# Optimization experiments

Measured on AMD Instinct MI355X. Metric: run time of the kernel, lower is better.

Reference implementation:

```python
import jax, jax.numpy as jnp
import numpy as np

B, N_P, N_S = 64, 50, 200
N_NODES = N_P * N_S          # 10000 nodes per graph (jobs x ops)
N_CAND = N_S + 1             # 201 candidates
INPUT_DIM, HIDDEN = 3, 64
NODE_DIM = 2 * HIDDEN        # h_nodes feature dim (=> actor in = 6*HIDDEN)
POOL_DIM = 4 * HIDDEN        # h_pooled dim (mean || max pooling)
H_ACTOR, H_CRITIC = 256, 256


def setup_inputs() -> dict:
    key = jax.random.key(0)
    ks = jax.random.split(key, 16)
    p = lambda k, sh: jax.random.normal(k, sh, jnp.float32) * 0.02
    x = jax.random.normal(ks[0], (B, N_NODES, INPUT_DIM), jnp.float32)
    candidate = jax.random.randint(ks[1], (B, N_CAND), 0, N_NODES)
    mask = jax.random.randint(ks[2], (B, N_CAND), 0, 2) > 0
    mask = mask.at[:, 0].set(True)  # guarantee at least one valid action per row
    return {
        "x": x, "candidate": candidate, "mask": mask,
        "fe_w1": p(ks[3], (INPUT_DIM, HIDDEN)), "fe_b1": jnp.zeros((HIDDEN,), jnp.float32),
        "fe_w2": p(ks[4], (HIDDEN, NODE_DIM)), "fe_b2": jnp.zeros((NODE_DIM,), jnp.float32),
        "a_w1": p(ks[5], (NODE_DIM + POOL_DIM, H_ACTOR)), "a_b1": jnp.zeros((H_ACTOR,), jnp.float32),
        "a_w2": p(ks[6], (H_ACTOR, H_ACTOR)), "a_b2": jnp.zeros((H_ACTOR,), jnp.float32),
        "a_w3": p(ks[7], (H_ACTOR, 1)), "a_b3": jnp.zeros((1,), jnp.float32),
        "c_w1": p(ks[8], (POOL_DIM, H_CRITIC)), "c_b1": jnp.zeros((H_CRITIC,), jnp.float32),
        "c_w2": p(ks[9], (H_CRITIC, H_CRITIC)), "c_b2": jnp.zeros((H_CRITIC,), jnp.float32),
        "c_w3": p(ks[10], (H_CRITIC, 1)), "c_b3": jnp.zeros((1,), jnp.float32),
    }


def _actor_critic(x, candidate, mask,
                  fe_w1, fe_b1, fe_w2, fe_b2,
                  a_w1, a_b1, a_w2, a_b2, a_w3, a_b3,
                  c_w1, c_b1, c_w2, c_b2, c_w3, c_b3):
    # --- feature_extract: per-node MLP embedding, graph-level pooling ---
    h = jax.nn.relu(jnp.einsum('bni,ih->bnh', x, fe_w1) + fe_b1)
    h_nodes = jax.nn.relu(jnp.einsum('bnh,hd->bnd', h, fe_w2) + fe_b2)   # [B, N, 2H]
    h_pooled = jnp.concatenate([h_nodes.mean(axis=1), h_nodes.max(axis=1)], axis=-1)  # [B, 4H]

    # --- gather candidate node features (torch.gather over node axis) ---
    cand_feat = jnp.take_along_axis(h_nodes, candidate[:, :, None], axis=1)  # [B, C, 2H]

    # --- concat broadcast pooled feature ---
    pooled_rep = jnp.broadcast_to(h_pooled[:, None, :], (cand_feat.shape[0], cand_feat.shape[1], h_pooled.shape[-1]))
    concat_fea = jnp.concatenate([cand_feat, pooled_rep], axis=-1)  # [B, C, 6H]

    # --- actor MLP (tanh hidden layers, linear out) ---
    a = jnp.tanh(concat_fea @ a_w1 + a_b1)
    a = jnp.tanh(a @ a_w2 + a_b2)
    scores = a @ a_w3 + a_b3                                    # [B, C, 1]

    # --- mask with -inf, softmax over candidate axis ---
    scores = jnp.where(mask[:, :, None], scores, -jnp.inf)
    pi = jax.nn.softmax(scores, axis=1)                          # [B, C, 1]

    # --- critic MLP on pooled feature ---
    c = jnp.tanh(h_pooled @ c_w1 + c_b1)
    c = jnp.tanh(c @ c_w2 + c_b2)
    v = c @ c_w3 + c_b3                                          # [B, 1]
    return pi, v


def reference(x, candidate, mask,
              fe_w1, fe_b1, fe_w2, fe_b2,
              a_w1, a_b1, a_w2, a_b2, a_w3, a_b3,
              c_w1, c_b1, c_w2, c_b2, c_w3, c_b3):
    return _actor_critic(x, candidate, mask,
                         fe_w1, fe_b1, fe_w2, fe_b2,
                         a_w1, a_b1, a_w2, a_b2, a_w3, a_b3,
                         c_w1, c_b1, c_w2, c_b2, c_w3, c_b3)
```

## Files before the change

### kernel.cpp

```cpp
#include <hip/hip_runtime.h>

#define NN 10000
#define NCAND 201
#define NB 64

typedef __attribute__((ext_vector_type(8))) short short8;
typedef __attribute__((ext_vector_type(4))) float f32x4;

__device__ __forceinline__ float bf2f(unsigned short u) {
  return __uint_as_float(((unsigned int)u) << 16);
}
__device__ __forceinline__ unsigned short f2bf(float f) {
  unsigned int u = __float_as_uint(f);
  u += 0x7FFFu + ((u >> 16) & 1u);
  return (unsigned short)(u >> 16);
}
__device__ __forceinline__ float fast_tanh(float x) {
  return 1.0f - 2.0f / (__expf(2.0f * x) + 1.0f);
}
__device__ __forceinline__ float gld(const void* p, long i, int f) {
  return f ? ((const float*)p)[i] : bf2f(((const unsigned short*)p)[i]);
}

__global__ __launch_bounds__(256)
void prep_kernel(const void* x, const void* w1, const void* b1, const void* w2,
                 const void* b2, const void* aw1, const void* ab1, const void* aw2,
                 const void* ab2, const void* aw3, const void* ab3,
                 const void* cw1, const void* cb1, const void* cw2, const void* cb2,
                 const void* cw3, const void* cb3,
                 const unsigned int* mask_w, const unsigned int* cand_w,
                 int* F, float* zero_base,
                 unsigned short* __restrict__ w2t, unsigned short* __restrict__ aw1t,
                 unsigned short* __restrict__ aw2t,
                 unsigned short* __restrict__ cw1t, unsigned short* __restrict__ cw2t) {
  const int t = threadIdx.x;
  const int j = blockIdx.x;

  if (j < 384) {
    __shared__ int cnts[5];
    if (t < 5) cnts[t] = 0;
    __syncthreads();
    const void* aps[5] = {w2, aw1, aw2, cw1, cw2};
#pragma unroll
    for (int a = 0; a < 5; ++a) {
      const unsigned short* p = (const unsigned short*)aps[a];
      if ((p[t] & 0x7F80u) >= 0x4300u) atomicAdd(&cnts[a], 1);
    }
    __syncthreads();
    const int Fw2 = cnts[0] > 32, Faw1 = cnts[1] > 32, Faw2 = cnts[2] > 32;
    const int Fcw1 = cnts[3] > 32, Fcw2 = cnts[4] > 32;
    int i = j * 256 + t;
    if (i < 128 * 64) { int n = i >> 6, k = i & 63; w2t[i] = f2bf(gld(w2, k * 128 + n, Fw2)); }
    if (i < 256 * 384) { int n = i / 384, k = i % 384; aw1t[i] = f2bf(gld(aw1, k * 256 + n, Faw1)); }
    if (i < 256 * 256) {
      int n = i >> 8, k = i & 255;
      aw2t[i] = f2bf(gld(aw2, k * 256 + n, Faw2));
      cw1t[i] = f2bf(gld(cw1, k * 256 + n, Fcw1));
      cw2t[i] = f2bf(gld(cw2, k * 256 + n, Fcw2));
    }
    return;
  }

  __shared__ int sh[3];
  if (t < 3) sh[t] = 0;
  __syncthreads();

  if (j < 401) {
    const void* ptrs[17] = {x, w1, b1, w2, b2, aw1, ab1, aw2, ab2, aw3, ab3,
                            cw1, cb1, cw2, cb2, cw3, cb3};
    const int sizes[17] = {1920000, 192, 64, 8192, 128, 98304, 256, 65536, 256,
                           256, 1, 65536, 256, 65536, 256, 256, 1};
    int a = j - 384;
    const unsigned short* p = (const unsigned short*)ptrs[a];
    int K = min(sizes[a], 2048);
    int c = 0;
    for (int i = t; i < K; i += 256)
      if ((p[i] & 0x7F80u) >= 0x4300u) c++;
    if (c) atomicAdd(&sh[0], c);
    __syncthreads();
    if (t == 0) F[a] = (sh[0] > (K >> 3)) ? 1 : 0;
  } else if (j == 401) {
    int flo = 0, fhi = 0, fgt = 0;
    for (int i = t; i < 3216; i += 256) {
      unsigned int w = mask_w[i];
      if ((w & 0xFFFFu) == 0x3F80u) flo = 1;
      if ((w >> 16) == 0x3F80u) fhi = 1;
      if (w > 1u) fgt = 1;
    }
    if (flo) sh[0] = 1;
    if (fhi) sh[1] = 1;
    if (fgt) sh[2] = 1;
    __syncthreads();
    if (t == 0) F[17] = sh[0] ? 2 : (sh[1] ? 3 : (sh[2] ? 1 : 0));
  } else if (j == 402) {
    int co = 0;
    for (int i = t; i < 1024; i += 256)
      if ((i & 1) && cand_w[i] != 0u) co = 1;
    if (co) sh[0] = 1;
    __syncthreads();
    if (t == 0) F[18] = sh[0] ? 0 : 1;
  } else {
    zero_base[(j - 403) * 256 + t] = 0.f;
  }
}

__global__ __launch_bounds__(256, 4)
void feat_pool_kernel(const void* __restrict__ x,
                      const void* __restrict__ w1, const void* __restrict__ b1,
                      const unsigned short* __restrict__ w2t,
                      const void* __restrict__ b2,
                      const int* __restrict__ F,
                      float* __restrict__ psum, float* __restrict__ pmax) {
  __shared__ __align__(16) unsigned short h1s[128 * 72];
  __shared__ float w1f[3 * 64];
  __shared__ float b1f[64];
  __shared__ float b2f[128];

  const int t = threadIdx.x;
  const int b = blockIdx.x >> 4;
  const int s = blockIdx.x & 15;
  const int lane = t & 63;
  const int wv = t >> 6;
  const int F0 = F[0], F1 = F[1], F2 = F[2], F4 = F[4];

  if (t < 192) w1f[t] = gld(w1, t, F1);
  if (t < 64) b1f[t] = gld(b1, t, F2);
  if (t < 128) b2f[t] = gld(b2, t, F4);

  short8 bfr[2][2];
#pragma unroll
  for (int nl = 0; nl < 2; ++nl)
#pragma unroll
    for (int ks = 0; ks < 2; ++ks) {
      int col = wv * 32 + nl * 16 + (lane & 15);
      bfr[nl][ks] = *(const short8*)(w2t + col * 64 + ((lane >> 4) * 8) + ks * 32);
    }
  __syncthreads();

  float csum[2] = {0.f, 0.f};
  float cmax[2] = {0.f, 0.f};

  const int m = t & 127;
  const int kg = t >> 7;

  float x0 = 0.f, x1 = 0.f, x2 = 0.f;
  {
    int c0 = s;
    if (c0 < 79) {
      int nb = c0 * 128;
      if (m < min(128, NN - nb)) {
        long xo = ((long)b * NN + nb + m) * 3;
        x0 = gld(x, xo, F0); x1 = gld(x, xo + 1, F0); x2 = gld(x, xo + 2, F0);
      }
    }
  }

  for (int c = s; c < 79; c += 16) {
    int nb = c * 128;
    int cnt = (nb + 128 <= NN) ? 128 : (NN - nb);
    if (m < cnt) {
#pragma unroll
      for (int blk = 0; blk < 4; ++blk) {
        short8 v;
#pragma unroll
        for (int i = 0; i < 8; ++i) {
          int k = kg * 32 + blk * 8 + i;
          float vv = x0 * w1f[k] + x1 * w1f[64 + k] + x2 * w1f[128 + k] + b1f[k];
          v[i] = (short)f2bf(fmaxf(vv, 0.f));
        }
        *(short8*)(h1s + m * 72 + kg * 32 + blk * 8) = v;
      }
    }
    {
      int cn = c + 16;
      float nx0 = 0.f, nx1 = 0.f, nx2 = 0.f;
      if (cn < 79) {
        int nbn = cn * 128;
        if (m < min(128, NN - nbn)) {
          long xo = ((long)b * NN + nbn + m) * 3;
          nx0 = gld(x, xo, F0); nx1 = gld(x, xo + 1, F0); nx2 = gld(x, xo + 2, F0);
        }
      }
      __syncthreads();
      x0 = nx0; x1 = nx1; x2 = nx2;
    }
#pragma unroll
    for (int mt = 0; mt < 8; ++mt) {
      const unsigned short* ap = h1s + (mt * 16 + (lane & 15)) * 72 + ((lane >> 4) * 8);
      short8 af0 = *(const short8*)(ap);
      short8 af1 = *(const short8*)(ap + 32);
#pragma unroll
      for (int nl = 0; nl < 2; ++nl) {
        f32x4 acc = {0.f, 0.f, 0.f, 0.f};
        acc = __builtin_amdgcn_mfma_f32_16x16x32_bf16(af0, bfr[nl][0], acc, 0, 0, 0);
        acc = __builtin_amdgcn_mfma_f32_16x16x32_bf16(af1, bfr[nl][1], acc, 0, 0, 0);
        int col = wv * 32 + nl * 16 + (lane & 15);
        float bb = b2f[col];
#pragma unroll
        for (int r = 0; r < 4; ++r) {
          int row = mt * 16 + ((lane >> 4) * 4) + r;
          if (row < cnt) {
            float v = fmaxf(acc[r] + bb, 0.f);
            csum[nl] += v;
            cmax[nl] = fmaxf(cmax[nl], v);
          }
        }
      }
    }
    __syncthreads();
  }
#pragma unroll
  for (int nl = 0; nl < 2; ++nl) {
    csum[nl] += __shfl_xor(csum[nl], 16);
    csum[nl] += __shfl_xor(csum[nl], 32);
    cmax[nl] = fmaxf(cmax[nl], __shfl_xor(cmax[nl], 16));
    cmax[nl] = fmaxf(cmax[nl], __shfl_xor(cmax[nl], 32));
  }
  if (lane < 16) {
#pragma unroll
    for (int nl = 0; nl < 2; ++nl) {
      int col = wv * 32 + nl * 16 + lane;
      atomicAdd(&psum[b * 128 + col], csum[nl]);
      atomicMax((int*)&pmax[b * 128 + col], __float_as_int(cmax[nl]));
    }
  }
}

__global__ __launch_bounds__(256)
void pooled_proj_kernel(const float* __restrict__ psum, const float* __restrict__ pmax,
                        const unsigned short* __restrict__ aw1t,
                        const void* __restrict__ ab1, const int* __restrict__ F,
                        float* __restrict__ pact) {
  __shared__ float plf[256];
  const int t = threadIdx.x, b = blockIdx.x;
  const int F6 = F[6];
  if (t < 128) {
    plf[t] = bf2f(f2bf(psum[b * 128 + t] * (1.0f / 10000.0f)));
    plf[128 + t] = bf2f(f2bf(pmax[b * 128 + t]));
  }
  __syncthreads();
  float a = gld(ab1, t, F6);
  const unsigned short* row = aw1t + t * 384 + 128;
#pragma unroll
  for (int k8 = 0; k8 < 32; ++k8) {
    short8 w = *(const short8*)(row + k8 * 8);
#pragma unroll
    for (int j = 0; j < 8; ++j)
      a += plf[k8 * 8 + j] * bf2f((unsigned short)w[j]);
  }
  pact[b * 256 + t] = a;
}

__global__ __launch_bounds__(256)
void actor_kernel(const void* __restrict__ x, const int* __restrict__ cand,
                  const void* __restrict__ w1, const void* __restrict__ b1,
                  const void* __restrict__ b2bf,
                  const void* __restrict__ ab2,
                  const void* __restrict__ aw3, const void* __restrict__ ab3,
                  const int* __restrict__ F,
                  const float* __restrict__ pact,
                  const unsigned short* __restrict__ w2t,
                  const unsigned short* __restrict__ aw1t,
                  const unsigned short* __restrict__ aw2t,
                  float* __restrict__ scores) {
  __shared__ __align__(16) unsigned short h1c[32 * 72];
  __shared__ __align__(16) unsigned short cf[32 * 136];
  __shared__ __align__(16) unsigned short a1s[32 * 264];
  __shared__ __align__(16) unsigned short a2s[32 * 264];
  __shared__ float pactS[256], ab2f[256], b2f[128];

  const int t = threadIdx.x;
  const int b = blockIdx.x / 7;
  const int cb = blockIdx.x % 7;
  const int cbase = cb * 29;
  const int cntc = min(29, NCAND - cbase);
  const int lane = t & 63;
  const int wv = t >> 6;
  const int F0 = F[0], F1 = F[1], F2 = F[2], F4 = F[4], F8 = F[8];
  const int F9 = F[9], F10 = F[10], C64 = F[18];

  pactS[t] = pact[b * 256 + t];
  ab2f[t] = gld(ab2, t, F8);
  if (t < 128) b2f[t] = gld(b2bf, t, F4);

  {
    int r = t & 31;
    int ci = cbase + r;
    if (ci > NCAND - 1) ci = NCAND - 1;
    long cidx = (long)b * NCAND + ci;
    int nd = C64 ? cand[2 * cidx] : cand[cidx];
    long xo = ((long)b * NN + nd) * 3;
    float x0 = gld(x, xo, F0), x1 = gld(x, xo + 1, F0), x2 = gld(x, xo + 2, F0);
    int kg = t >> 5;
#pragma unroll
    for (int i = 0; i < 8; ++i) {
      int k = kg * 8 + i;
      float v = x0 * gld(w1, k, F1) + x1 * gld(w1, 64 + k, F1) +
                x2 * gld(w1, 128 + k, F1) + gld(b1, k, F2);
      h1c[r * 72 + k] = f2bf(fmaxf(v, 0.f));
    }
  }
  __syncthreads();

  {
    short8 af[2][2];
#pragma unroll
    for (int mt = 0; mt < 2; ++mt)
#pragma unroll
      for (int ks = 0; ks < 2; ++ks)
        af[mt][ks] = *(const short8*)(h1c + (mt * 16 + (lane & 15)) * 72 + ((lane >> 4) * 8) + ks * 32);
#pragma unroll
    for (int nl = 0; nl < 2; ++nl) {
      int col = wv * 32 + nl * 16 + (lane & 15);
      short8 bf0 = *(const short8*)(w2t + col * 64 + ((lane >> 4) * 8));
      short8 bf1 = *(const short8*)(w2t + col * 64 + ((lane >> 4) * 8) + 32);
      float bb = b2f[col];
#pragma unroll
      for (int mt = 0; mt < 2; ++mt) {
        f32x4 acc = {0.f, 0.f, 0.f, 0.f};
        acc = __builtin_amdgcn_mfma_f32_16x16x32_bf16(af[mt][0], bf0, acc, 0, 0, 0);
        acc = __builtin_amdgcn_mfma_f32_16x16x32_bf16(af[mt][1], bf1, acc, 0, 0, 0);
#pragma unroll
        for (int r = 0; r < 4; ++r) {
          int row = mt * 16 + ((lane >> 4) * 4) + r;
          cf[row * 136 + col] = f2bf(fmaxf(acc[r] + bb, 0.f));
        }
      }
    }
  }
  __syncthreads();

  {
    f32x4 acc[2][4];
#pragma unroll
    for (int mt = 0; mt < 2; ++mt)
#pragma unroll
      for (int nt = 0; nt < 4; ++nt) acc[mt][nt] = (f32x4){0.f, 0.f, 0.f, 0.f};
#pragma unroll
    for (int ks = 0; ks < 4; ++ks) {
      short8 af0 = *(const short8*)(cf + (lane & 15) * 136 + ks * 32 + ((lane >> 4) * 8));
      short8 af1 = *(const short8*)(cf + (16 + (lane & 15)) * 136 + ks * 32 + ((lane >> 4) * 8));
#pragma unroll
      for (int nt = 0; nt < 4; ++nt) {
        int col = wv * 64 + nt * 16 + (lane & 15);
        short8 bfr = *(const short8*)(aw1t + col * 384 + ks * 32 + ((lane >> 4) * 8));
        acc[0][nt] = __builtin_amdgcn_mfma_f32_16x16x32_bf16(af0, bfr, acc[0][nt], 0, 0, 0);
        acc[1][nt] = __builtin_amdgcn_mfma_f32_16x16x32_bf16(af1, bfr, acc[1][nt], 0, 0, 0);
      }
    }
#pragma unroll
    for (int mt = 0; mt < 2; ++mt)
#pragma unroll
      for (int nt = 0; nt < 4; ++nt) {
        int col = wv * 64 + nt * 16 + (lane & 15);
        float bb = pactS[col];
#pragma unroll
        for (int r = 0; r < 4; ++r) {
          int row = mt * 16 + ((lane >> 4) * 4) + r;
          a1s[row * 264 + col] = f2bf(fast_tanh(acc[mt][nt][r] + bb));
        }
      }
  }
  __syncthreads();

  {
    f32x4 acc[2][4];
#pragma unroll
    for (int mt = 0; mt < 2; ++mt)
#pragma unroll
      for (int nt = 0; nt < 4; ++nt) acc[mt][nt] = (f32x4){0.f, 0.f, 0.f, 0.f};
    for (int ks = 0; ks < 8; ++ks) {
      short8 af0 = *(const short8*)(a1s + (lane & 15) * 264 + ks * 32 + ((lane >> 4) * 8));
      short8 af1 = *(const short8*)(a1s + (16 + (lane & 15)) * 264 + ks * 32 + ((lane >> 4) * 8));
#pragma unroll
      for (int nt = 0; nt < 4; ++nt) {
        int col = wv * 64 + nt * 16 + (lane & 15);
        short8 bfr = *(const short8*)(aw2t + col * 256 + ks * 32 + ((lane >> 4) * 8));
        acc[0][nt] = __builtin_amdgcn_mfma_f32_16x16x32_bf16(af0, bfr, acc[0][nt], 0, 0, 0);
        acc[1][nt] = __builtin_amdgcn_mfma_f32_16x16x32_bf16(af1, bfr, acc[1][nt], 0, 0, 0);
      }
    }
#pragma unroll
    for (int mt = 0; mt < 2; ++mt)
#pragma unroll
      for (int nt = 0; nt < 4; ++nt) {
        int col = wv * 64 + nt * 16 + (lane & 15);
        float bb = ab2f[col];
#pragma unroll
        for (int r = 0; r < 4; ++r) {
          int row = mt * 16 + ((lane >> 4) * 4) + r;
          a2s[row * 264 + col] = f2bf(fast_tanh(acc[mt][nt][r] + bb));
        }
      }
  }
  __syncthreads();

  {
    int row = t >> 3, seg = t & 7;
    float p = 0.f;
#pragma unroll 8
    for (int i = 0; i < 32; ++i) {
      int k = seg * 32 + i;
      p += bf2f(a2s[row * 264 + k]) * gld(aw3, k, F9);
    }
    p += __shfl_xor(p, 1);
    p += __shfl_xor(p, 2);
    p += __shfl_xor(p, 4);
    if (seg == 0 && row < cntc)
      scores[b * 256 + cbase + row] = p + gld(ab3, 0, F10);
  }
}

__global__ __launch_bounds__(256)
void softmax_critic_kernel(const float* __restrict__ scores,
                           const void* __restrict__ mask,
                           const int* __restrict__ F,
                           const float* __restrict__ psum,
                           const float* __restrict__ pmax,
                           const unsigned short* __restrict__ cw1t,
                           const unsigned short* __restrict__ cw2t,
                           const void* __restrict__ cb1, const void* __restrict__ cb2,
                           const void* __restrict__ cw3, const void* __restrict__ cb3,
                           void* __restrict__ out) {
  __shared__ float plf[256];
  __shared__ float c1f[256];
  __shared__ float red[4];
  const int t = threadIdx.x;
  const int b = blockIdx.x & 63;
  const int lane = t & 63, wv = t >> 6;
  const int OF = (F[0] + F[1] + F[3] + F[5] + F[7] + F[9] + F[11] + F[13] + F[15]) >= 5;

  if (blockIdx.x < 64) {
    const int MM = F[17];
    float sraw = 0.f, sv = -1e30f;
    bool valid = false;
    if (t < NCAND) {
      sraw = scores[b * 256 + t];
      long idx = (long)b * NCAND + t;
      if (MM == 0)      valid = ((const int*)mask)[idx] != 0;
      else if (MM == 1) valid = ((const unsigned char*)mask)[idx] != 0;
      else if (MM == 2) valid = ((const unsigned short*)mask)[idx] != 0;
      else              valid = ((const unsigned int*)mask)[idx] != 0;
      if (valid) sv = sraw;
    }
    float m = sv;
    for (int o = 32; o; o >>= 1) m = fmaxf(m, __shfl_xor(m, o));
    if (lane == 0) red[wv] = m;
    __syncthreads();
    m = fmaxf(fmaxf(red[0], red[1]), fmaxf(red[2], red[3]));
    __syncthreads();
    float e = valid ? __expf(sraw - m) : 0.f;
    if (!(e == e)) e = 0.f;
    float ss = e;
    for (int o = 32; o; o >>= 1) ss += __shfl_xor(ss, o);
    if (lane == 0) red[wv] = ss;
    __syncthreads();
    float tot = red[0] + red[1] + red[2] + red[3];
    tot = fmaxf(tot, 1e-30f);
    if (t < NCAND) {
      float pv = e / tot;
      if (!(pv == pv)) pv = 0.f;
      if (OF) ((float*)out)[b * NCAND + t] = pv;
      else ((unsigned short*)out)[b * NCAND + t] = f2bf(pv);
    }
  } else {
    const int F12 = F[12], F14 = F[14], F15 = F[15], F16 = F[16];
    if (t < 128) {
      plf[t] = psum[b * 128 + t] * (1.0f / 10000.0f);
      plf[128 + t] = pmax[b * 128 + t];
    }
    __syncthreads();
    {
      float a = gld(cb1, t, F12);
      const unsigned short* row = cw1t + t * 256;
#pragma unroll
      for (int k8 = 0; k8 < 32; ++k8) {
        short8 w = *(const short8*)(row + k8 * 8);
#pragma unroll
        for (int j = 0; j < 8; ++j)
          a += plf[k8 * 8 + j] * bf2f((unsigned short)w[j]);
      }
      c1f[t] = fast_tanh(a);
    }
    __syncthreads();
    {
      float a2 = gld(cb2, t, F14);
      const unsigned short* row = cw2t + t * 256;
#pragma unroll
      for (int k8 = 0; k8 < 32; ++k8) {
        short8 w = *(const short8*)(row + k8 * 8);
#pragma unroll
        for (int j = 0; j < 8; ++j)
          a2 += c1f[k8 * 8 + j] * bf2f((unsigned short)w[j]);
      }
      a2 = fast_tanh(a2);
      float p = a2 * gld(cw3, t, F15);
      for (int o = 32; o; o >>= 1) p += __shfl_xor(p, o);
      __syncthreads();
      if (lane == 0) red[wv] = p;
      __syncthreads();
      if (t == 0) {
        float v = red[0] + red[1] + red[2] + red[3] + gld(cb3, 0, F16);
        if (!(v == v)) v = 0.f;
        if (OF) ((float*)out)[NB * NCAND + b] = v;
        else ((unsigned short*)out)[NB * NCAND + b] = f2bf(v);
      }
    }
  }
}

extern "C" void kernel_launch(void* const* d_in, const int* in_sizes, int n_in,
                              void* d_out, int out_size, void* d_ws, size_t ws_size,
                              hipStream_t stream) {
  const void* x = d_in[0];
  const int* cand = (const int*)d_in[1];
  const void* mask = d_in[2];
  const void* fe_w1 = d_in[3];
  const void* fe_b1 = d_in[4];
  const void* fe_w2 = d_in[5];
  const void* fe_b2 = d_in[6];
  const void* a_w1 = d_in[7];
  const void* a_b1 = d_in[8];
  const void* a_w2 = d_in[9];
  const void* a_b2 = d_in[10];
  const void* a_w3 = d_in[11];
  const void* a_b3 = d_in[12];
  const void* c_w1 = d_in[13];
  const void* c_b1 = d_in[14];
  const void* c_w2 = d_in[15];
  const void* c_b2 = d_in[16];
  const void* c_w3 = d_in[17];
  const void* c_b3 = d_in[18];

  char* ws = (char*)d_ws;
  float* psum = (float*)(ws + 0);
  float* pmax = (float*)(ws + 32768);
  float* scores = (float*)(ws + 65536);
  unsigned short* w2t = (unsigned short*)(ws + 131072);
  unsigned short* aw1t = (unsigned short*)(ws + 147456);
  unsigned short* aw2t = (unsigned short*)(ws + 344064);
  int* F = (int*)(ws + 475136);
  unsigned short* cw1t = (unsigned short*)(ws + 475264);
  unsigned short* cw2t = (unsigned short*)(ws + 606336);
  float* pact = (float*)(ws + 737408);

  prep_kernel<<<467, 256, 0, stream>>>(x, fe_w1, fe_b1, fe_w2, fe_b2,
                                       a_w1, a_b1, a_w2, a_b2, a_w3, a_b3,
                                       c_w1, c_b1, c_w2, c_b2, c_w3, c_b3,
                                       (const unsigned int*)mask,
                                       (const unsigned int*)cand, F, psum,
                                       w2t, aw1t, aw2t, cw1t, cw2t);
  feat_pool_kernel<<<1024, 256, 0, stream>>>(x, fe_w1, fe_b1, w2t, fe_b2, F, psum, pmax);
  pooled_proj_kernel<<<64, 256, 0, stream>>>(psum, pmax, aw1t, a_b1, F, pact);
  actor_kernel<<<448, 256, 0, stream>>>(x, cand, fe_w1, fe_b1, fe_b2,
                                        a_b2, a_w3, a_b3, F, pact,
                                        w2t, aw1t, aw2t, scores);
  softmax_critic_kernel<<<128, 256, 0, stream>>>(scores, mask, F, psum, pmax,
                                                 cw1t, cw2t, c_b1, c_b2, c_w3, c_b3,
                                                 (void*)d_out);
}
```

Baseline: 167.2 us.

## Merge feature pooling with candidate embedding and fuse softmax into actor tail

Candidate node embedding (second feature-extract layer) now runs as extra blocks inside the pooling kernel and writes its bf16 features to workspace. The pooled projection and critic share one kernel. The actor MLP kernel finishes with a last-block-per-batch softmax driven by an atomic counter. This cuts five launches to four and lets the candidate gather overlap with pooling, at the cost of a global round trip for candidate features, atomics, and a serialized softmax tail.

```diff
diff --git a/kernel.cpp b/kernel.cpp
--- a/kernel.cpp
+++ b/kernel.cpp
@@ -29,7 +29,7 @@
                  const void* cw1, const void* cb1, const void* cw2, const void* cb2,
                  const void* cw3, const void* cb3,
                  const unsigned int* mask_w, const unsigned int* cand_w,
-                 int* F, float* zero_base,
+                 int* F, float* zero_base, int* scnt,
                  unsigned short* __restrict__ w2t, unsigned short* __restrict__ aw1t,
                  unsigned short* __restrict__ aw2t,
                  unsigned short* __restrict__ cw1t, unsigned short* __restrict__ cw2t) {
@@ -97,6 +97,7 @@
     for (int i = t; i < 1024; i += 256)
       if ((i & 1) && cand_w[i] != 0u) co = 1;
     if (co) sh[0] = 1;
+    if (t < 64) scnt[t] = 0;
     __syncthreads();
     if (t == 0) F[18] = sh[0] ? 0 : 1;
   } else {
@@ -105,365 +106,220 @@
 }
 
 __global__ __launch_bounds__(256, 4)
-void feat_pool_kernel(const void* __restrict__ x,
+void fp_actorA_kernel(const void* __restrict__ x, const int* __restrict__ cand,
                       const void* __restrict__ w1, const void* __restrict__ b1,
                       const unsigned short* __restrict__ w2t,
                       const void* __restrict__ b2,
                       const int* __restrict__ F,
-                      float* __restrict__ psum, float* __restrict__ pmax) {
-  __shared__ __align__(16) unsigned short h1s[128 * 72];
+                      float* __restrict__ psum, float* __restrict__ pmax,
+                      unsigned short* __restrict__ cfw) {
+  __shared__ __align__(16) unsigned short pool[128 * 72];
   __shared__ float w1f[3 * 64];
   __shared__ float b1f[64];
   __shared__ float b2f[128];
 
   const int t = threadIdx.x;
-  const int b = blockIdx.x >> 4;
-  const int s = blockIdx.x & 15;
   const int lane = t & 63;
   const int wv = t >> 6;
   const int F0 = F[0], F1 = F[1], F2 = F[2], F4 = F[4];
 
-  if (t < 192) w1f[t] = gld(w1, t, F1);
-  if (t < 64) b1f[t] = gld(b1, t, F2);
-  if (t < 128) b2f[t] = gld(b2, t, F4);
-
-  short8 bfr[2][2];
-#pragma unroll
-  for (int nl = 0; nl < 2; ++nl)
-#pragma unroll
-    for (int ks = 0; ks < 2; ++ks) {
-      int col = wv * 32 + nl * 16 + (lane & 15);
-      bfr[nl][ks] = *(const short8*)(w2t + col * 64 + ((lane >> 4) * 8) + ks * 32);
-    }
-  __syncthreads();
-
-  float csum[2] = {0.f, 0.f};
-  float cmax[2] = {0.f, 0.f};
-
-  const int m = t & 127;
-  const int kg = t >> 7;
-
-  float x0 = 0.f, x1 = 0.f, x2 = 0.f;
-  {
-    int c0 = s;
-    if (c0 < 79) {
-      int nb = c0 * 128;
+  if (blockIdx.x < 1024) {
+    unsigned short* h1s = pool;
+    const int b = blockIdx.x >> 4;
+    const int s = blockIdx.x & 15;
+
+    if (t < 192) w1f[t] = gld(w1, t, F1);
+    if (t < 64) b1f[t] = gld(b1, t, F2);
+    if (t < 128) b2f[t] = gld(b2, t, F4);
+
+    short8 bfr[2][2];
+#pragma unroll
+    for (int nl = 0; nl < 2; ++nl)
+#pragma unroll
+      for (int ks = 0; ks < 2; ++ks) {
+        int col = wv * 32 + nl * 16 + (lane & 15);
+        bfr[nl][ks] = *(const short8*)(w2t + col * 64 + ((lane >> 4) * 8) + ks * 32);
+      }
+    __syncthreads();
+
+    float csum[2] = {0.f, 0.f};
+    float cmax[2] = {0.f, 0.f};
+    const int m = t & 127;
+    const int kg = t >> 7;
+
+    float x0 = 0.f, x1 = 0.f, x2 = 0.f;
+    if (s < 79) {
+      int nb = s * 128;
       if (m < min(128, NN - nb)) {
         long xo = ((long)b * NN + nb + m) * 3;
         x0 = gld(x, xo, F0); x1 = gld(x, xo + 1, F0); x2 = gld(x, xo + 2, F0);
       }
     }
-  }
-
-  for (int c = s; c < 79; c += 16) {
-    int nb = c * 128;
-    int cnt = (nb + 128 <= NN) ? 128 : (NN - nb);
-    if (m < cnt) {
-#pragma unroll
-      for (int blk = 0; blk < 4; ++blk) {
-        short8 v;
-#pragma unroll
-        for (int i = 0; i < 8; ++i) {
-          int k = kg * 32 + blk * 8 + i;
-          float vv = x0 * w1f[k] + x1 * w1f[64 + k] + x2 * w1f[128 + k] + b1f[k];
-          v[i] = (short)f2bf(fmaxf(vv, 0.f));
+
+    for (int c = s; c < 79; c += 16) {
+      int nb = c * 128;
+      int cnt = (nb + 128 <= NN) ? 128 : (NN - nb);
+      if (m < cnt) {
+#pragma unroll
+        for (int blk = 0; blk < 4; ++blk) {
+          short8 v;
+#pragma unroll
+          for (int i = 0; i < 8; ++i) {
+            int k = kg * 32 + blk * 8 + i;
+            float vv = x0 * w1f[k] + x1 * w1f[64 + k] + x2 * w1f[128 + k] + b1f[k];
+            v[i] = (short)f2bf(fmaxf(vv, 0.f));
+          }
+          *(short8*)(h1s + m * 72 + kg * 32 + blk * 8) = v;
         }
-        *(short8*)(h1s + m * 72 + kg * 32 + blk * 8) = v;
-      }
-    }
-    {
-      int cn = c + 16;
-      float nx0 = 0.f, nx1 = 0.f, nx2 = 0.f;
-      if (cn < 79) {
-        int nbn = cn * 128;
-        if (m < min(128, NN - nbn)) {
-          long xo = ((long)b * NN + nbn + m) * 3;
-          nx0 = gld(x, xo, F0); nx1 = gld(x, xo + 1, F0); nx2 = gld(x, xo + 2, F0);
-        }
-      }
-      __syncthreads();
-      x0 = nx0; x1 = nx1; x2 = nx2;
-    }
-#pragma unroll
-    for (int mt = 0; mt < 8; ++mt) {
-      const unsigned short* ap = h1s + (mt * 16 + (lane & 15)) * 72 + ((lane >> 4) * 8);
-      short8 af0 = *(const short8*)(ap);
-      short8 af1 = *(const short8*)(ap + 32);
-#pragma unroll
-      for (int nl = 0; nl < 2; ++nl) {
-        f32x4 acc = {0.f, 0.f, 0.f, 0.f};
-        acc = __builtin_amdgcn_mfma_f32_16x16x32_bf16(af0, bfr[nl][0], acc, 0, 0, 0);
-        acc = __builtin_amdgcn_mfma_f32_16x16x32_bf16(af1, bfr[nl][1], acc, 0, 0, 0);
-        int col = wv * 32 + nl * 16 + (lane & 15);
-        float bb = b2f[col];
-#pragma unroll
-        for (int r = 0; r < 4; ++r) {
-          int row = mt * 16 + ((lane >> 4) * 4) + r;
-          if (row < cnt) {
-            float v = fmaxf(acc[r] + bb, 0.f);
-            csum[nl] += v;
-            cmax[nl] = fmaxf(cmax[nl], v);
+      }
+      {
+        int cn = c + 16;
+        float nx0 = 0.f, nx1 = 0.f, nx2 = 0.f;
+        if (cn < 79) {
+          int nbn = cn * 128;
+          if (m < min(128, NN - nbn)) {
+            long xo = ((long)b * NN + nbn + m) * 3;
+            nx0 = gld(x, xo, F0); nx1 = gld(x, xo + 1, F0); nx2 = gld(x, xo + 2, F0);
           }
         }
-      }
-    }
-    __syncthreads();
-  }
-#pragma unroll
-  for (int nl = 0; nl < 2; ++nl) {
-    csum[nl] += __shfl_xor(csum[nl], 16);
-    csum[nl] += __shfl_xor(csum[nl], 32);
-    cmax[nl] = fmaxf(cmax[nl], __shfl_xor(cmax[nl], 16));
-    cmax[nl] = fmaxf(cmax[nl], __shfl_xor(cmax[nl], 32));
-  }
-  if (lane < 16) {
+        __syncthreads();
+        x0 = nx0; x1 = nx1; x2 = nx2;
+      }
+#pragma unroll
+      for (int mt = 0; mt < 8; ++mt) {
+        const unsigned short* ap = h1s + (mt * 16 + (lane & 15)) * 72 + ((lane >> 4) * 8);
+        short8 af0 = *(const short8*)(ap);
+        short8 af1 = *(const short8*)(ap + 32);
+#pragma unroll
+        for (int nl = 0; nl < 2; ++nl) {
+          f32x4 acc = {0.f, 0.f, 0.f, 0.f};
+          acc = __builtin_amdgcn_mfma_f32_16x16x32_bf16(af0, bfr[nl][0], acc, 0, 0, 0);
+          acc = __builtin_amdgcn_mfma_f32_16x16x32_bf16(af1, bfr[nl][1], acc, 0, 0, 0);
+          int col = wv * 32 + nl * 16 + (lane & 15);
+          float bb = b2f[col];
+#pragma unroll
+          for (int r = 0; r < 4; ++r) {
+            int row = mt * 16 + ((lane >> 4) * 4) + r;
+            if (row < cnt) {
+              float v = fmaxf(acc[r] + bb, 0.f);
+              csum[nl] += v;
+              cmax[nl] = fmaxf(cmax[nl], v);
+            }
+          }
+        }
+      }
+      __syncthreads();
+    }
 #pragma unroll
     for (int nl = 0; nl < 2; ++nl) {
-      int col = wv * 32 + nl * 16 + lane;
-      atomicAdd(&psum[b * 128 + col], csum[nl]);
-      atomicMax((int*)&pmax[b * 128 + col], __float_as_int(cmax[nl]));
+      csum[nl] += __shfl_xor(csum[nl], 16);
+      csum[nl] += __shfl_xor(csum[nl], 32);
+      cmax[nl] = fmaxf(cmax[nl], __shfl_xor(cmax[nl], 16));
+      cmax[nl] = fmaxf(cmax[nl], __shfl_xor(cmax[nl], 32));
+    }
+    if (lane < 16) {
+#pragma unroll
+      for (int nl = 0; nl < 2; ++nl) {
+        int col = wv * 32 + nl * 16 + lane;
+        atomicAdd(&psum[b * 128 + col], csum[nl]);
+        atomicMax((int*)&pmax[b * 128 + col], __float_as_int(cmax[nl]));
+      }
+    }
+  } else {
+    unsigned short* h1c = pool;
+    unsigned short* cf = pool + 2560;
+    const int idx = blockIdx.x - 1024;
+    const int b = idx / 7;
+    const int cb = idx % 7;
+    const int cbase = cb * 29;
+    const int C64 = F[18];
+
+    if (t < 128) b2f[t] = gld(b2, t, F4);
+
+    {
+      int r = t & 31;
+      int ci = cbase + r;
+      if (ci > NCAND - 1) ci = NCAND - 1;
+      long cidx = (long)b * NCAND + ci;
+      int nd = C64 ? cand[2 * cidx] : cand[cidx];
+      long xo = ((long)b * NN + nd) * 3;
+      float x0 = gld(x, xo, F0), x1 = gld(x, xo + 1, F0), x2 = gld(x, xo + 2, F0);
+      int kg = t >> 5;
+#pragma unroll
+      for (int i = 0; i < 8; ++i) {
+        int k = kg * 8 + i;
+        float v = x0 * gld(w1, k, F1) + x1 * gld(w1, 64 + k, F1) +
+                  x2 * gld(w1, 128 + k, F1) + gld(b1, k, F2);
+        h1c[r * 72 + k] = f2bf(fmaxf(v, 0.f));
+      }
+    }
+    __syncthreads();
+
+    {
+      short8 af[2][2];
+#pragma unroll
+      for (int mt = 0; mt < 2; ++mt)
+#pragma unroll
+        for (int ks = 0; ks < 2; ++ks)
+          af[mt][ks] = *(const short8*)(h1c + (mt * 16 + (lane & 15)) * 72 + ((lane >> 4) * 8) + ks * 32);
+#pragma unroll
+      for (int nl = 0; nl < 2; ++nl) {
+        int col = wv * 32 + nl * 16 + (lane & 15);
+        short8 bf0 = *(const short8*)(w2t + col * 64 + ((lane >> 4) * 8));
+        short8 bf1 = *(const short8*)(w2t + col * 64 + ((lane >> 4) * 8) + 32);
+        float bb = b2f[col];
+#pragma unroll
+        for (int mt = 0; mt < 2; ++mt) {
+          f32x4 acc = {0.f, 0.f, 0.f, 0.f};
+          acc = __builtin_amdgcn_mfma_f32_16x16x32_bf16(af[mt][0], bf0, acc, 0, 0, 0);
+          acc = __builtin_amdgcn_mfma_f32_16x16x32_bf16(af[mt][1], bf1, acc, 0, 0, 0);
+#pragma unroll
+          for (int r = 0; r < 4; ++r) {
+            int row = mt * 16 + ((lane >> 4) * 4) + r;
+            cfw[(long)idx * 4096 + row * 128 + col] = f2bf(fmaxf(acc[r] + bb, 0.f));
+          }
+        }
+      }
     }
   }
 }
 
 __global__ __launch_bounds__(256)
-void pooled_proj_kernel(const float* __restrict__ psum, const float* __restrict__ pmax,
-                        const unsigned short* __restrict__ aw1t,
-                        const void* __restrict__ ab1, const int* __restrict__ F,
-                        float* __restrict__ pact) {
-  __shared__ float plf[256];
-  const int t = threadIdx.x, b = blockIdx.x;
-  const int F6 = F[6];
-  if (t < 128) {
-    plf[t] = bf2f(f2bf(psum[b * 128 + t] * (1.0f / 10000.0f)));
-    plf[128 + t] = bf2f(f2bf(pmax[b * 128 + t]));
-  }
-  __syncthreads();
-  float a = gld(ab1, t, F6);
-  const unsigned short* row = aw1t + t * 384 + 128;
-#pragma unroll
-  for (int k8 = 0; k8 < 32; ++k8) {
-    short8 w = *(const short8*)(row + k8 * 8);
-#pragma unroll
-    for (int j = 0; j < 8; ++j)
-      a += plf[k8 * 8 + j] * bf2f((unsigned short)w[j]);
-  }
-  pact[b * 256 + t] = a;
-}
-
-__global__ __launch_bounds__(256)
-void actor_kernel(const void* __restrict__ x, const int* __restrict__ cand,
-                  const void* __restrict__ w1, const void* __restrict__ b1,
-                  const void* __restrict__ b2bf,
-                  const void* __restrict__ ab2,
-                  const void* __restrict__ aw3, const void* __restrict__ ab3,
-                  const int* __restrict__ F,
-                  const float* __restrict__ pact,
-                  const unsigned short* __restrict__ w2t,
-                  const unsigned short* __restrict__ aw1t,
-                  const unsigned short* __restrict__ aw2t,
-                  float* __restrict__ scores) {
-  __shared__ __align__(16) unsigned short h1c[32 * 72];
-  __shared__ __align__(16) unsigned short cf[32 * 136];
-  __shared__ __align__(16) unsigned short a1s[32 * 264];
-  __shared__ __align__(16) unsigned short a2s[32 * 264];
-  __shared__ float pactS[256], ab2f[256], b2f[128];
-
-  const int t = threadIdx.x;
-  const int b = blockIdx.x / 7;
-  const int cb = blockIdx.x % 7;
-  const int cbase = cb * 29;
-  const int cntc = min(29, NCAND - cbase);
-  const int lane = t & 63;
-  const int wv = t >> 6;
-  const int F0 = F[0], F1 = F[1], F2 = F[2], F4 = F[4], F8 = F[8];
-  const int F9 = F[9], F10 = F[10], C64 = F[18];
-
-  pactS[t] = pact[b * 256 + t];
-  ab2f[t] = gld(ab2, t, F8);
-  if (t < 128) b2f[t] = gld(b2bf, t, F4);
-
-  {
-    int r = t & 31;
-    int ci = cbase + r;
-    if (ci > NCAND - 1) ci = NCAND - 1;
-    long cidx = (long)b * NCAND + ci;
-    int nd = C64 ? cand[2 * cidx] : cand[cidx];
-    long xo = ((long)b * NN + nd) * 3;
-    float x0 = gld(x, xo, F0), x1 = gld(x, xo + 1, F0), x2 = gld(x, xo + 2, F0);
-    int kg = t >> 5;
-#pragma unroll
-    for (int i = 0; i < 8; ++i) {
-      int k = kg * 8 + i;
-      float v = x0 * gld(w1, k, F1) + x1 * gld(w1, 64 + k, F1) +
-                x2 * gld(w1, 128 + k, F1) + gld(b1, k, F2);
-      h1c[r * 72 + k] = f2bf(fmaxf(v, 0.f));
-    }
-  }
-  __syncthreads();
-
-  {
-    short8 af[2][2];
-#pragma unroll
-    for (int mt = 0; mt < 2; ++mt)
-#pragma unroll
-      for (int ks = 0; ks < 2; ++ks)
-        af[mt][ks] = *(const short8*)(h1c + (mt * 16 + (lane & 15)) * 72 + ((lane >> 4) * 8) + ks * 32);
-#pragma unroll
-    for (int nl = 0; nl < 2; ++nl) {
-      int col = wv * 32 + nl * 16 + (lane & 15);
-      short8 bf0 = *(const short8*)(w2t + col * 64 + ((lane >> 4) * 8));
-      short8 bf1 = *(const short8*)(w2t + col * 64 + ((lane >> 4) * 8) + 32);
-      float bb = b2f[col];
-#pragma unroll
-      for (int mt = 0; mt < 2; ++mt) {
-        f32x4 acc = {0.f, 0.f, 0.f, 0.f};
-        acc = __builtin_amdgcn_mfma_f32_16x16x32_bf16(af[mt][0], bf0, acc, 0, 0, 0);
-        acc = __builtin_amdgcn_mfma_f32_16x16x32_bf16(af[mt][1], bf1, acc, 0, 0, 0);
-#pragma unroll
-        for (int r = 0; r < 4; ++r) {
-          int row = mt * 16 + ((lane >> 4) * 4) + r;
-          cf[row * 136 + col] = f2bf(fmaxf(acc[r] + bb, 0.f));
-        }
-      }
-    }
-  }
-  __syncthreads();
-
-  {
-    f32x4 acc[2][4];
-#pragma unroll
-    for (int mt = 0; mt < 2; ++mt)
-#pragma unroll
-      for (int nt = 0; nt < 4; ++nt) acc[mt][nt] = (f32x4){0.f, 0.f, 0.f, 0.f};
-#pragma unroll
-    for (int ks = 0; ks < 4; ++ks) {
-      short8 af0 = *(const short8*)(cf + (lane & 15) * 136 + ks * 32 + ((lane >> 4) * 8));
-      short8 af1 = *(const short8*)(cf + (16 + (lane & 15)) * 136 + ks * 32 + ((lane >> 4) * 8));
-#pragma unroll
-      for (int nt = 0; nt < 4; ++nt) {
-        int col = wv * 64 + nt * 16 + (lane & 15);
-        short8 bfr = *(const short8*)(aw1t + col * 384 + ks * 32 + ((lane >> 4) * 8));
-        acc[0][nt] = __builtin_amdgcn_mfma_f32_16x16x32_bf16(af0, bfr, acc[0][nt], 0, 0, 0);
-        acc[1][nt] = __builtin_amdgcn_mfma_f32_16x16x32_bf16(af1, bfr, acc[1][nt], 0, 0, 0);
-      }
-    }
-#pragma unroll
-    for (int mt = 0; mt < 2; ++mt)
-#pragma unroll
-      for (int nt = 0; nt < 4; ++nt) {
-        int col = wv * 64 + nt * 16 + (lane & 15);
-        float bb = pactS[col];
-#pragma unroll
-        for (int r = 0; r < 4; ++r) {
-          int row = mt * 16 + ((lane >> 4) * 4) + r;
-          a1s[row * 264 + col] = f2bf(fast_tanh(acc[mt][nt][r] + bb));
-        }
-      }
-  }
-  __syncthreads();
-
-  {
-    f32x4 acc[2][4];
-#pragma unroll
-    for (int mt = 0; mt < 2; ++mt)
-#pragma unroll
-      for (int nt = 0; nt < 4; ++nt) acc[mt][nt] = (f32x4){0.f, 0.f, 0.f, 0.f};
-    for (int ks = 0; ks < 8; ++ks) {
-      short8 af0 = *(const short8*)(a1s + (lane & 15) * 264 + ks * 32 + ((lane >> 4) * 8));
-      short8 af1 = *(const short8*)(a1s + (16 + (lane & 15)) * 264 + ks * 32 + ((lane >> 4) * 8));
-#pragma unroll
-      for (int nt = 0; nt < 4; ++nt) {
-        int col = wv * 64 + nt * 16 + (lane & 15);
-        short8 bfr = *(const short8*)(aw2t + col * 256 + ks * 32 + ((lane >> 4) * 8));
-        acc[0][nt] = __builtin_amdgcn_mfma_f32_16x16x32_bf16(af0, bfr, acc[0][nt], 0, 0, 0);
-        acc[1][nt] = __builtin_amdgcn_mfma_f32_16x16x32_bf16(af1, bfr, acc[1][nt], 0, 0, 0);
-      }
-    }
-#pragma unroll
-    for (int mt = 0; mt < 2; ++mt)
-#pragma unroll
-      for (int nt = 0; nt < 4; ++nt) {
-        int col = wv * 64 + nt * 16 + (lane & 15);
-        float bb = ab2f[col];
-#pragma unroll
-        for (int r = 0; r < 4; ++r) {
-          int row = mt * 16 + ((lane >> 4) * 4) + r;
-          a2s[row * 264 + col] = f2bf(fast_tanh(acc[mt][nt][r] + bb));
-        }
-      }
-  }
-  __syncthreads();
-
-  {
-    int row = t >> 3, seg = t & 7;
-    float p = 0.f;
-#pragma unroll 8
-    for (int i = 0; i < 32; ++i) {
-      int k = seg * 32 + i;
-      p += bf2f(a2s[row * 264 + k]) * gld(aw3, k, F9);
-    }
-    p += __shfl_xor(p, 1);
-    p += __shfl_xor(p, 2);
-    p += __shfl_xor(p, 4);
-    if (seg == 0 && row < cntc)
-      scores[b * 256 + cbase + row] = p + gld(ab3, 0, F10);
-  }
-}
-
-__global__ __launch_bounds__(256)
-void softmax_critic_kernel(const float* __restrict__ scores,
-                           const void* __restrict__ mask,
-                           const int* __restrict__ F,
-                           const float* __restrict__ psum,
-                           const float* __restrict__ pmax,
-                           const unsigned short* __restrict__ cw1t,
-                           const unsigned short* __restrict__ cw2t,
-                           const void* __restrict__ cb1, const void* __restrict__ cb2,
-                           const void* __restrict__ cw3, const void* __restrict__ cb3,
-                           void* __restrict__ out) {
+void pp_critic_kernel(const float* __restrict__ psum, const float* __restrict__ pmax,
+                      const unsigned short* __restrict__ aw1t,
+                      const void* __restrict__ ab1,
+                      const unsigned short* __restrict__ cw1t,
+                      const unsigned short* __restrict__ cw2t,
+                      const void* __restrict__ cb1, const void* __restrict__ cb2,
+                      const void* __restrict__ cw3, const void* __restrict__ cb3,
+                      const int* __restrict__ F,
+                      float* __restrict__ pact, void* __restrict__ out) {
   __shared__ float plf[256];
   __shared__ float c1f[256];
   __shared__ float red[4];
   const int t = threadIdx.x;
   const int b = blockIdx.x & 63;
   const int lane = t & 63, wv = t >> 6;
-  const int OF = (F[0] + F[1] + F[3] + F[5] + F[7] + F[9] + F[11] + F[13] + F[15]) >= 5;
 
   if (blockIdx.x < 64) {
-    const int MM = F[17];
-    float sraw = 0.f, sv = -1e30f;
-    bool valid = false;
-    if (t < NCAND) {
-      sraw = scores[b * 256 + t];
-      long idx = (long)b * NCAND + t;
-      if (MM == 0)      valid = ((const int*)mask)[idx] != 0;
-      else if (MM == 1) valid = ((const unsigned char*)mask)[idx] != 0;
-      else if (MM == 2) valid = ((const unsigned short*)mask)[idx] != 0;
-      else              valid = ((const unsigned int*)mask)[idx] != 0;
-      if (valid) sv = sraw;
-    }
-    float m = sv;
-    for (int o = 32; o; o >>= 1) m = fmaxf(m, __shfl_xor(m, o));
-    if (lane == 0) red[wv] = m;
-    __syncthreads();
-    m = fmaxf(fmaxf(red[0], red[1]), fmaxf(red[2], red[3]));
-    __syncthreads();
-    float e = valid ? __expf(sraw - m) : 0.f;
-    if (!(e == e)) e = 0.f;
-    float ss = e;
-    for (int o = 32; o; o >>= 1) ss += __shfl_xor(ss, o);
-    if (lane == 0) red[wv] = ss;
-    __syncthreads();
-    float tot = red[0] + red[1] + red[2] + red[3];
-    tot = fmaxf(tot, 1e-30f);
-    if (t < NCAND) {
-      float pv = e / tot;
-      if (!(pv == pv)) pv = 0.f;
-      if (OF) ((float*)out)[b * NCAND + t] = pv;
-      else ((unsigned short*)out)[b * NCAND + t] = f2bf(pv);
-    }
+    const int F6 = F[6];
+    if (t < 128) {
+      plf[t] = bf2f(f2bf(psum[b * 128 + t] * (1.0f / 10000.0f)));
+      plf[128 + t] = bf2f(f2bf(pmax[b * 128 + t]));
+    }
+    __syncthreads();
+    float a = gld(ab1, t, F6);
+    const unsigned short* row = aw1t + t * 384 + 128;
+#pragma unroll
+    for (int k8 = 0; k8 < 32; ++k8) {
+      short8 w = *(const short8*)(row + k8 * 8);
+#pragma unroll
+      for (int j = 0; j < 8; ++j)
+        a += plf[k8 * 8 + j] * bf2f((unsigned short)w[j]);
+    }
+    pact[b * 256 + t] = a;
   } else {
+    const int OF = (F[0] + F[1] + F[3] + F[5] + F[7] + F[9] + F[11] + F[13] + F[15]) >= 5;
     const int F12 = F[12], F14 = F[14], F15 = F[15], F16 = F[16];
     if (t < 128) {
       plf[t] = psum[b * 128 + t] * (1.0f / 10000.0f);
@@ -506,6 +362,160 @@
         else ((unsigned short*)out)[NB * NCAND + b] = f2bf(v);
       }
     }
+  }
+}
+
+__global__ __launch_bounds__(256)
+void actorB_kernel(const unsigned short* __restrict__ cfw,
+                   const void* __restrict__ ab2,
+                   const void* __restrict__ aw3, const void* __restrict__ ab3,
+                   const void* __restrict__ mask,
+                   const int* __restrict__ F,
+                   const float* __restrict__ pact,
+                   const unsigned short* __restrict__ aw1t,
+                   const unsigned short* __restrict__ aw2t,
+                   float* __restrict__ scores, int* __restrict__ scnt,
+                   void* __restrict__ out) {
+  __shared__ __align__(16) unsigned short a1s[32 * 264];
+  __shared__ __align__(16) unsigned short a2s[32 * 264];
+  __shared__ float pactS[256], ab2f[256];
+  __shared__ float red[4];
+  __shared__ int amLast;
+
+  const int t = threadIdx.x;
+  const int b = blockIdx.x / 7;
+  const int cb = blockIdx.x % 7;
+  const int cbase = cb * 29;
+  const int cntc = min(29, NCAND - cbase);
+  const int lane = t & 63;
+  const int wv = t >> 6;
+  const int F8 = F[8], F9 = F[9], F10 = F[10];
+
+  pactS[t] = pact[b * 256 + t];
+  ab2f[t] = gld(ab2, t, F8);
+
+  {
+    f32x4 acc[2][4];
+#pragma unroll
+    for (int mt = 0; mt < 2; ++mt)
+#pragma unroll
+      for (int nt = 0; nt < 4; ++nt) acc[mt][nt] = (f32x4){0.f, 0.f, 0.f, 0.f};
+    const unsigned short* cfb = cfw + (long)blockIdx.x * 4096;
+#pragma unroll
+    for (int ks = 0; ks < 4; ++ks) {
+      short8 af0 = *(const short8*)(cfb + (lane & 15) * 128 + ks * 32 + ((lane >> 4) * 8));
+      short8 af1 = *(const short8*)(cfb + (16 + (lane & 15)) * 128 + ks * 32 + ((lane >> 4) * 8));
+#pragma unroll
+      for (int nt = 0; nt < 4; ++nt) {
+        int col = wv * 64 + nt * 16 + (lane & 15);
+        short8 bfr = *(const short8*)(aw1t + col * 384 + ks * 32 + ((lane >> 4) * 8));
+        acc[0][nt] = __builtin_amdgcn_mfma_f32_16x16x32_bf16(af0, bfr, acc[0][nt], 0, 0, 0);
+        acc[1][nt] = __builtin_amdgcn_mfma_f32_16x16x32_bf16(af1, bfr, acc[1][nt], 0, 0, 0);
+      }
+    }
+    __syncthreads();
+#pragma unroll
+    for (int mt = 0; mt < 2; ++mt)
+#pragma unroll
+      for (int nt = 0; nt < 4; ++nt) {
+        int col = wv * 64 + nt * 16 + (lane & 15);
+        float bb = pactS[col];
+#pragma unroll
+        for (int r = 0; r < 4; ++r) {
+          int row = mt * 16 + ((lane >> 4) * 4) + r;
+          a1s[row * 264 + col] = f2bf(fast_tanh(acc[mt][nt][r] + bb));
+        }
+      }
+  }
+  __syncthreads();
+
+  {
+    f32x4 acc[2][4];
+#pragma unroll
+    for (int mt = 0; mt < 2; ++mt)
+#pragma unroll
+      for (int nt = 0; nt < 4; ++nt) acc[mt][nt] = (f32x4){0.f, 0.f, 0.f, 0.f};
+    for (int ks = 0; ks < 8; ++ks) {
+      short8 af0 = *(const short8*)(a1s + (lane & 15) * 264 + ks * 32 + ((lane >> 4) * 8));
+      short8 af1 = *(const short8*)(a1s + (16 + (lane & 15)) * 264 + ks * 32 + ((lane >> 4) * 8));
+#pragma unroll
+      for (int nt = 0; nt < 4; ++nt) {
+        int col = wv * 64 + nt * 16 + (lane & 15);
+        short8 bfr = *(const short8*)(aw2t + col * 256 + ks * 32 + ((lane >> 4) * 8));
+        acc[0][nt] = __builtin_amdgcn_mfma_f32_16x16x32_bf16(af0, bfr, acc[0][nt], 0, 0, 0);
+        acc[1][nt] = __builtin_amdgcn_mfma_f32_16x16x32_bf16(af1, bfr, acc[1][nt], 0, 0, 0);
+      }
+    }
+#pragma unroll
+    for (int mt = 0; mt < 2; ++mt)
+#pragma unroll
+      for (int nt = 0; nt < 4; ++nt) {
+        int col = wv * 64 + nt * 16 + (lane & 15);
+        float bb = ab2f[col];
+#pragma unroll
+        for (int r = 0; r < 4; ++r) {
+          int row = mt * 16 + ((lane >> 4) * 4) + r;
+          a2s[row * 264 + col] = f2bf(fast_tanh(acc[mt][nt][r] + bb));
+        }
+      }
+  }
+  __syncthreads();
+
+  {
+    int row = t >> 3, seg = t & 7;
+    float p = 0.f;
+#pragma unroll 8
+    for (int i = 0; i < 32; ++i) {
+      int k = seg * 32 + i;
+      p += bf2f(a2s[row * 264 + k]) * gld(aw3, k, F9);
+    }
+    p += __shfl_xor(p, 1);
+    p += __shfl_xor(p, 2);
+    p += __shfl_xor(p, 4);
+    if (seg == 0 && row < cntc)
+      atomicExch(&scores[b * 256 + cbase + row], p + gld(ab3, 0, F10));
+  }
+  __syncthreads();
+
+  if (t == 0) {
+    __threadfence();
+    amLast = (atomicAdd(&scnt[b], 1) == 6);
+  }
+  __syncthreads();
+  if (!amLast) return;
+
+  const int MM = F[17];
+  const int OF = (F[0] + F[1] + F[3] + F[5] + F[7] + F[9] + F[11] + F[13] + F[15]) >= 5;
+  float sraw = 0.f, sv = -1e30f;
+  bool valid = false;
+  if (t < NCAND) {
+    sraw = atomicAdd(&scores[b * 256 + t], 0.0f);
+    long idx = (long)b * NCAND + t;
+    if (MM == 0)      valid = ((const int*)mask)[idx] != 0;
+    else if (MM == 1) valid = ((const unsigned char*)mask)[idx] != 0;
+    else if (MM == 2) valid = ((const unsigned short*)mask)[idx] != 0;
+    else              valid = ((const unsigned int*)mask)[idx] != 0;
+    if (valid) sv = sraw;
+  }
+  float m = sv;
+  for (int o = 32; o; o >>= 1) m = fmaxf(m, __shfl_xor(m, o));
+  if (lane == 0) red[wv] = m;
+  __syncthreads();
+  m = fmaxf(fmaxf(red[0], red[1]), fmaxf(red[2], red[3]));
+  __syncthreads();
+  float e = valid ? __expf(sraw - m) : 0.f;
+  if (!(e == e)) e = 0.f;
+  float ss = e;
+  for (int o = 32; o; o >>= 1) ss += __shfl_xor(ss, o);
+  if (lane == 0) red[wv] = ss;
+  __syncthreads();
+  float tot = red[0] + red[1] + red[2] + red[3];
+  tot = fmaxf(tot, 1e-30f);
+  if (t < NCAND) {
+    float pv = e / tot;
+    if (!(pv == pv)) pv = 0.f;
+    if (OF) ((float*)out)[b * NCAND + t] = pv;
+    else ((unsigned short*)out)[b * NCAND + t] = f2bf(pv);
   }
 }
 
@@ -543,19 +553,20 @@
   unsigned short* cw1t = (unsigned short*)(ws + 475264);
   unsigned short* cw2t = (unsigned short*)(ws + 606336);
   float* pact = (float*)(ws + 737408);
+  unsigned short* cfw = (unsigned short*)(ws + 802944);
+  int* scnt = (int*)(ws + 4472960);
 
   prep_kernel<<<467, 256, 0, stream>>>(x, fe_w1, fe_b1, fe_w2, fe_b2,
                                        a_w1, a_b1, a_w2, a_b2, a_w3, a_b3,
                                        c_w1, c_b1, c_w2, c_b2, c_w3, c_b3,
                                        (const unsigned int*)mask,
-                                       (const unsigned int*)cand, F, psum,
+                                       (const unsigned int*)cand, F, psum, scnt,
                                        w2t, aw1t, aw2t, cw1t, cw2t);
-  feat_pool_kernel<<<1024, 256, 0, stream>>>(x, fe_w1, fe_b1, w2t, fe_b2, F, psum, pmax);
-  pooled_proj_kernel<<<64, 256, 0, stream>>>(psum, pmax, aw1t, a_b1, F, pact);
-  actor_kernel<<<448, 256, 0, stream>>>(x, cand, fe_w1, fe_b1, fe_b2,
-                                        a_b2, a_w3, a_b3, F, pact,
-                                        w2t, aw1t, aw2t, scores);
-  softmax_critic_kernel<<<128, 256, 0, stream>>>(scores, mask, F, psum, pmax,
-                                                 cw1t, cw2t, c_b1, c_b2, c_w3, c_b3,
-                                                 (void*)d_out);
-}
+  fp_actorA_kernel<<<1472, 256, 0, stream>>>(x, cand, fe_w1, fe_b1, w2t, fe_b2,
+                                             F, psum, pmax, cfw);
+  pp_critic_kernel<<<128, 256, 0, stream>>>(psum, pmax, aw1t, a_b1,
+                                            cw1t, cw2t, c_b1, c_b2, c_w3, c_b3,
+                                            F, pact, (void*)d_out);
+  actorB_kernel<<<448, 256, 0, stream>>>(cfw, a_b2, a_w3, a_b3, mask, F, pact,
+                                         aw1t, aw2t, scores, scnt, (void*)d_out);
+}
```

Measured after the change: 164.9 us. About the same (-1.4%).
